# Kernel optimization log

Measured on AMD Instinct MI355X. Metric: run time of the kernel, lower is better.

Reference implementation:

```python
import jax, jax.numpy as jnp
import numpy as np

B = 256      # graph pairs
N = 256      # nodes per graph (uniform -> padding is a reshape)
DEG = 16     # avg degree
D = 32       # one_hot_dim
F1, F2, F3 = 128, 64, 64
T = 16       # tensor_neurons
BINS = 16
BOT = 16     # bottle_neck_neurons


def setup_inputs() -> dict:
    key = jax.random.key(0)
    ks = jax.random.split(key, 24)
    NT = B * N            # total nodes per side
    NE = B * N * DEG      # total directed edges per side
    x_q = jax.random.normal(ks[0], (NT, D), jnp.float32)
    x_c = jax.random.normal(ks[1], (NT, D), jnp.float32)
    edge_q = jax.random.randint(ks[2], (2, NE), 0, NT, jnp.int32)
    edge_c = jax.random.randint(ks[3], (2, NE), 0, NT, jnp.int32)
    qgraph_sizes = jnp.full((B,), N, jnp.int32)
    cgraph_sizes = jnp.full((B,), N, jnp.int32)

    def glorot(k, shape):
        fan = sum(shape[-2:]) if len(shape) >= 2 else shape[0] * 2
        return jax.random.uniform(k, shape, jnp.float32, -1.0, 1.0) * np.sqrt(6.0 / fan)

    params = dict(
        W1=glorot(ks[4], (D, F1)), b1=jnp.zeros((F1,), jnp.float32),
        W2=glorot(ks[5], (F1, F2)), b2=jnp.zeros((F2,), jnp.float32),
        W3=glorot(ks[6], (F2, F3)), b3=jnp.zeros((F3,), jnp.float32),
        attn_w=glorot(ks[7], (F3, F3)),
        ntn_a_w=glorot(ks[8], (T, F3, F3)),
        ntn_b_w=glorot(ks[9], (2 * F3, T)),
        ntn_bias=glorot(ks[10], (T, 1)),
        fc1_w=glorot(ks[11], (T + BINS, BOT)), fc1_b=jnp.zeros((BOT,), jnp.float32),
        fc2_w=glorot(ks[12], (BOT, 1)), fc2_b=jnp.zeros((1,), jnp.float32),
    )
    return dict(x_q=x_q, edge_q=edge_q, x_c=x_c, edge_c=edge_c,
                qgraph_sizes=qgraph_sizes, cgraph_sizes=cgraph_sizes, **params)


def _gcn(x, src, dst, W, b):
    n = x.shape[0]
    h = x @ W
    loop = jnp.arange(n, dtype=src.dtype)
    s = jnp.concatenate([src, loop])
    d = jnp.concatenate([dst, loop])
    deg = jax.ops.segment_sum(jnp.ones(s.shape, h.dtype), d, num_segments=n)
    dinv = jnp.where(deg > 0, jax.lax.rsqrt(jnp.maximum(deg, 1.0)), 0.0)
    coef = (dinv[s] * dinv[d])[:, None]
    return jax.ops.segment_sum(h[s] * coef, d, num_segments=n) + b


def _gnn(x, ei, W1, b1, W2, b2, W3, b3):
    src, dst = ei[0], ei[1]
    h = jax.nn.relu(_gcn(x, src, dst, W1, b1))        # dropout is identity in eval
    h = jax.nn.relu(_gcn(h, src, dst, W2, b2))
    return _gcn(h, src, dst, W3, b3)                  # [B*N, F3]


def _att_pool(q, attn_w, sizes):
    # q: [B, N, F3]
    ctx = jnp.tanh((q.sum(axis=1) @ attn_w) / sizes.astype(q.dtype)[:, None])  # [B, F3]
    sig = jax.nn.sigmoid(jnp.einsum('bnf,bf->bn', q, ctx))                      # [B, N]
    return jnp.einsum('bnf,bn->bf', q, sig)                                     # [B, F3]


def _pair_hist(q, c):
    # per-pair histogram of q @ c^T with BINS bins over each pair's [min, max]
    s = jax.lax.stop_gradient(jnp.einsum('bnf,bmf->bnm', q, c))  # [B, N, N]
    mn = s.min(axis=(1, 2), keepdims=True)
    mx = s.max(axis=(1, 2), keepdims=True)
    idx = jnp.clip(jnp.floor((s - mn) / jnp.maximum(mx - mn, 1e-12) * BINS),
                   0, BINS - 1).astype(jnp.int32)
    gid = (idx + jnp.arange(B, dtype=jnp.int32)[:, None, None] * BINS).reshape(-1)
    h = jax.ops.segment_sum(jnp.ones(gid.shape, jnp.float32), gid,
                            num_segments=B * BINS).reshape(B, BINS)
    return h / h.sum(axis=1, keepdims=True)


def reference(x_q, edge_q, x_c, edge_c, qgraph_sizes, cgraph_sizes,
              W1, b1, W2, b2, W3, b3, attn_w, ntn_a_w, ntn_b_w, ntn_bias,
              fc1_w, fc1_b, fc2_w, fc2_b):
    q = _gnn(x_q, edge_q, W1, b1, W2, b2, W3, b3).reshape(B, N, F3)
    c = _gnn(x_c, edge_c, W1, b1, W2, b2, W3, b3).reshape(B, N, F3)
    e1 = _att_pool(q, attn_w, qgraph_sizes)
    e2 = _att_pool(c, attn_w, cgraph_sizes)
    ntn = (jnp.einsum('bi,tij,bj->bt', e1, ntn_a_w, e2)
           + jnp.concatenate([e1, e2], axis=-1) @ ntn_b_w
           + ntn_bias[:, 0])
    scores = jax.nn.relu(ntn)                                   # [B, T]
    hist = _pair_hist(q, c)                                     # [B, BINS]
    scores = jnp.concatenate([scores, hist], axis=1)
    scores = jax.nn.relu(scores @ fc1_w + fc1_b)
    p = jax.nn.sigmoid(scores @ fc2_w + fc2_b)[:, 0]            # [B]
    ged = -0.5 * (qgraph_sizes + cgraph_sizes).astype(p.dtype) * jnp.log(p)
    return ged
```

## Files before the change

### kernel.cpp

```cpp
#include <hip/hip_runtime.h>
#include <hip/hip_bf16.h>
#include <math.h>

#define BB 256
#define NN 256
#define NT (BB*NN)
#define NT2 (2*NT)
#define NE (NT*16)
#define DD 32
#define F1C 128
#define F2C 64
#define F3C 64
#define TT 16
#define BINS 16

#define NBUCK 256
#define BSHIFT 9
#define BNODES 512
#define BCAP 10240
#define EPB 4096

typedef __attribute__((ext_vector_type(8))) short short8;
typedef __attribute__((ext_vector_type(4))) float f32x4;
typedef __attribute__((ext_vector_type(2))) float f32x2;

__device__ inline float b2f(ushort u) { return __uint_as_float(((uint)u) << 16); }
__device__ inline ushort f2b(float f) {
    uint u = __float_as_uint(f);
    return (ushort)((u + 0x7fffu + ((u >> 16) & 1u)) >> 16);
}
__device__ inline float clamp8(float v) { return fminf(fmaxf(v, -448.0f), 448.0f); }
__device__ inline uchar f2f8(float v) {
    int r = __builtin_amdgcn_cvt_pk_fp8_f32(clamp8(v), 0.0f, 0, false);
    return (uchar)(r & 0xff);
}
__device__ inline void f8x8_acc(uint2 w, float* acc) {
    f32x2 p;
    p = __builtin_amdgcn_cvt_pk_f32_fp8(w.x, false); acc[0] += p.x; acc[1] += p.y;
    p = __builtin_amdgcn_cvt_pk_f32_fp8(w.x, true);  acc[2] += p.x; acc[3] += p.y;
    p = __builtin_amdgcn_cvt_pk_f32_fp8(w.y, false); acc[4] += p.x; acc[5] += p.y;
    p = __builtin_amdgcn_cvt_pk_f32_fp8(w.y, true);  acc[6] += p.x; acc[7] += p.y;
}
__device__ inline uint2 f8x8_pack(const float* v) {
    uint2 r;
    r.x = (uint)__builtin_amdgcn_cvt_pk_fp8_f32(clamp8(v[0]), clamp8(v[1]), 0, false);
    r.x = (uint)__builtin_amdgcn_cvt_pk_fp8_f32(clamp8(v[2]), clamp8(v[3]), (int)r.x, true);
    r.y = (uint)__builtin_amdgcn_cvt_pk_fp8_f32(clamp8(v[4]), clamp8(v[5]), 0, false);
    r.y = (uint)__builtin_amdgcn_cvt_pk_fp8_f32(clamp8(v[6]), clamp8(v[7]), (int)r.y, true);
    return r;
}

__global__ __launch_bounds__(256) void zero_k(int* __restrict__ gcount) {
    gcount[threadIdx.x] = 0;
}

__global__ __launch_bounds__(256) void p1cvt_k(const int* __restrict__ eq, const int* __restrict__ ec,
                                               uint* __restrict__ staged, int* __restrict__ gcount,
                                               const float* __restrict__ W1, const float* __restrict__ W2,
                                               const float* __restrict__ W3, ushort* __restrict__ Wt1,
                                               ushort* __restrict__ Wt2, uchar* __restrict__ Wt3f8) {
    int t = threadIdx.x;
    if (blockIdx.x < 512) {
        __shared__ uint s_pk[EPB];
        __shared__ int s_cnt[NBUCK];
        __shared__ int s_off[NBUCK];
        __shared__ int s_base[NBUCK];
        __shared__ int s_gb[NBUCK];
        bool sideB = blockIdx.x >= 256;
        const int* edge = sideB ? ec : eq;
        int off = sideB ? NT : 0;
        int e0 = (blockIdx.x & 255) * EPB;
        s_cnt[t] = 0;
        __syncthreads();
        uint pk[16]; int bk[16];
#pragma unroll
        for (int j = 0; j < 16; j++) {
            int e = e0 + j * 256 + t;
            int s = edge[e] + off;
            int d = edge[NE + e] + off;
            bk[j] = d >> BSHIFT;
            pk[j] = ((uint)s << BSHIFT) | (uint)(d & (BNODES - 1));
            atomicAdd(&s_cnt[bk[j]], 1);
        }
        __syncthreads();
        s_off[t] = s_cnt[t];
        __syncthreads();
        for (int o = 1; o < NBUCK; o <<= 1) {
            int x = (t >= o) ? s_off[t - o] : 0;
            __syncthreads();
            s_off[t] += x;
            __syncthreads();
        }
        {
            int ex = s_off[t] - s_cnt[t];
            s_base[t] = ex;
            s_off[t] = ex;
            s_gb[t] = atomicAdd(&gcount[t], s_cnt[t]);
        }
        __syncthreads();
#pragma unroll
        for (int j = 0; j < 16; j++) {
            int pos = atomicAdd(&s_off[bk[j]], 1);
            s_pk[pos] = pk[j];
        }
        __syncthreads();
        int w = t >> 6, l = t & 63;
        int bsel = l >> 4, l16 = l & 15;
        for (int pb = w; pb < NBUCK / 4; pb += 4) {
            int bkt = pb * 4 + bsel;
            int n = s_cnt[bkt], st = s_base[bkt], gb = s_gb[bkt];
            if (gb + n > BCAP) n = max(0, BCAP - gb);
            for (int i = l16; i < n; i += 16)
                staged[bkt * BCAP + gb + i] = s_pk[st + i];
        }
    } else {
        int i = (blockIdx.x - 512) * 256 + t;
        if (i < DD * F1C)  { int k = i / F1C, n = i % F1C; Wt1[n * DD + k]  = f2b(W1[i]); }
        if (i < F1C * F2C) { int k = i / F2C, n = i % F2C; Wt2[n * F1C + k] = f2b(W2[i]); }
        if (i < F2C * F3C) { int k = i / F3C, n = i % F3C; Wt3f8[n * F2C + k] = f2f8(W3[i]); }
    }
}

__global__ __launch_bounds__(256) void csr_p2_k(const uint* __restrict__ staged, const int* __restrict__ gcount,
                                                int* __restrict__ rp, int* __restrict__ indeg,
                                                float* __restrict__ dinv, int* __restrict__ ep,
                                                const float* __restrict__ xq, const float* __restrict__ xc,
                                                ushort* __restrict__ xb) {
    int b = blockIdx.x;
    int t = threadIdx.x;
    __shared__ int cnt[BNODES];
    __shared__ int fl[BNODES];
    __shared__ int wsum[256];
    __shared__ int gsc[NBUCK];
    __shared__ float sdv[BNODES];
    cnt[t] = 0; cnt[t + 256] = 0;
    gsc[t] = min(gcount[t], BCAP);
    __syncthreads();
    for (int off = 1; off < NBUCK; off <<= 1) {
        int x = (t >= off) ? gsc[t - off] : 0;
        __syncthreads();
        gsc[t] += x;
        __syncthreads();
    }
    int gbase = (b == 0) ? 0 : gsc[b - 1];
    int n = min(gcount[b], BCAP);
    const uint* sb = staged + (size_t)b * BCAP;
    int i = t;
    for (; i + 768 < n; i += 1024) {
        uint p0 = sb[i];
        uint p1 = sb[i + 256];
        uint p2 = sb[i + 512];
        uint p3 = sb[i + 768];
        atomicAdd(&cnt[p0 & (BNODES - 1)], 1);
        atomicAdd(&cnt[p1 & (BNODES - 1)], 1);
        atomicAdd(&cnt[p2 & (BNODES - 1)], 1);
        atomicAdd(&cnt[p3 & (BNODES - 1)], 1);
    }
    for (; i < n; i += 256)
        atomicAdd(&cnt[sb[i] & (BNODES - 1)], 1);
    __syncthreads();
    int base2 = t * 2;
    int c0 = cnt[base2], c1 = cnt[base2 + 1];
    int s2 = c0 + c1;
    wsum[t] = s2;
    __syncthreads();
    for (int off = 1; off < 256; off <<= 1) {
        int x = (t >= off) ? wsum[t - off] : 0;
        __syncthreads();
        wsum[t] += x;
        __syncthreads();
    }
    int p = gbase + wsum[t] - s2;
    int v0 = b * BNODES + base2;
    float d0 = rsqrtf((float)(c0 + 1));
    float d1 = rsqrtf((float)(c1 + 1));
    rp[v0] = p;          fl[base2] = p;
    indeg[v0] = c0;      dinv[v0] = d0;      sdv[base2] = d0;
    p += c0;
    rp[v0 + 1] = p;      fl[base2 + 1] = p;
    indeg[v0 + 1] = c1;  dinv[v0 + 1] = d1;  sdv[base2 + 1] = d1;
    __syncthreads();
    i = t;
    for (; i + 768 < n; i += 1024) {
        uint p0 = sb[i];
        uint p1 = sb[i + 256];
        uint p2 = sb[i + 512];
        uint p3 = sb[i + 768];
        ep[atomicAdd(&fl[p0 & (BNODES - 1)], 1)] = (int)(p0 >> BSHIFT);
        ep[atomicAdd(&fl[p1 & (BNODES - 1)], 1)] = (int)(p1 >> BSHIFT);
        ep[atomicAdd(&fl[p2 & (BNODES - 1)], 1)] = (int)(p2 >> BSHIFT);
        ep[atomicAdd(&fl[p3 & (BNODES - 1)], 1)] = (int)(p3 >> BSHIFT);
    }
    for (; i < n; i += 256) {
        uint pk = sb[i];
        ep[atomicAdd(&fl[pk & (BNODES - 1)], 1)] = (int)(pk >> BSHIFT);
    }
    {
        const float* xs = (b < 128) ? (xq + (size_t)b * BNODES * DD)
                                    : (xc + ((size_t)b * BNODES - NT) * DD);
        ushort* xd = xb + (size_t)b * BNODES * DD;
        for (int g = t; g < BNODES * DD / 4; g += 256) {
            int r = g >> 3;
            float4 v = ((const float4*)xs)[g];
            float dv = sdv[r];
            ushort4 o;
            o.x = f2b(v.x * dv); o.y = f2b(v.y * dv);
            o.z = f2b(v.z * dv); o.w = f2b(v.w * dv);
            ((ushort4*)xd)[g] = o;
        }
    }
}

__global__ __launch_bounds__(256) void l1_k(const ushort* __restrict__ xb,
                                            const ushort* __restrict__ Wt1,
                                            const float* __restrict__ b1,
                                            const ushort* __restrict__ Wt2,
                                            const int* __restrict__ rp,
                                            const int* __restrict__ indeg,
                                            const int* __restrict__ ep,
                                            const float* __restrict__ dinv,
                                            uchar* __restrict__ h8a) {
    __shared__ ushort s_x[64][40];
    __shared__ ushort s_h1[64][136];
    int t = threadIdx.x;
    size_t rows0 = (size_t)blockIdx.x * 64;

    {
        int gl = t >> 2;
        int l4 = t & 3;
        int v = (int)rows0 + gl;
        float dv = dinv[v];
        short8 rs = *(const short8*)(xb + (size_t)v * 32 + l4 * 8);
        float acc[8];
#pragma unroll
        for (int j = 0; j < 8; j++) acc[j] = b2f((ushort)rs[j]);
        int start = rp[v];
        int cnt   = indeg[v];
        int i = 0;
        for (; i + 8 <= cnt; i += 8) {
            int sx[8];
#pragma unroll
            for (int j = 0; j < 8; j++) sx[j] = ep[start + i + j];
            short8 r[8];
#pragma unroll
            for (int j = 0; j < 8; j++) r[j] = *(const short8*)(xb + (size_t)sx[j] * 32 + l4 * 8);
#pragma unroll
            for (int j = 0; j < 8; j++)
#pragma unroll
                for (int k = 0; k < 8; k++) acc[k] += b2f((ushort)r[j][k]);
        }
        for (; i < cnt; i++) {
            int s0 = ep[start + i];
            short8 r0 = *(const short8*)(xb + (size_t)s0 * 32 + l4 * 8);
#pragma unroll
            for (int j = 0; j < 8; j++) acc[j] += b2f((ushort)r0[j]);
        }
        short8 o;
#pragma unroll
        for (int j = 0; j < 8; j++) o[j] = (short)f2b(dv * acc[j]);
        *(short8*)&s_x[gl][l4 * 8] = o;
    }
    __syncthreads();

    int w = t >> 6, lane = t & 63;
    int r16 = lane & 15, quad = lane >> 4, koff = quad * 8;

    short8 af1 = *(const short8*)&s_x[w * 16 + r16][koff];
#pragma unroll
    for (int nt = 0; nt < 8; nt++) {
        short8 bfr = *(const short8*)(Wt1 + (size_t)(nt * 16 + r16) * 32 + koff);
        f32x4 acc = {0.f, 0.f, 0.f, 0.f};
        acc = __builtin_amdgcn_mfma_f32_16x16x32_bf16(af1, bfr, acc, 0, 0, 0);
        int col = nt * 16 + r16;
        float bc = b1[col];
#pragma unroll
        for (int r = 0; r < 4; r++) {
            int rl = w * 16 + quad * 4 + r;
            s_h1[rl][col] = f2b(fmaxf(acc[r] + bc, 0.0f));
        }
    }
    __syncthreads();

    short8 af2[4];
#pragma unroll
    for (int kc = 0; kc < 4; kc++)
        af2[kc] = *(const short8*)&s_h1[w * 16 + r16][kc * 32 + koff];
    float dvr[4];
#pragma unroll
    for (int r = 0; r < 4; r++)
        dvr[r] = dinv[rows0 + w * 16 + quad * 4 + r];
#pragma unroll
    for (int nt = 0; nt < 4; nt++) {
        f32x4 acc = {0.f, 0.f, 0.f, 0.f};
#pragma unroll
        for (int kc = 0; kc < 4; kc++) {
            short8 bfr = *(const short8*)(Wt2 + (size_t)(nt * 16 + r16) * 128 + kc * 32 + koff);
            acc = __builtin_amdgcn_mfma_f32_16x16x32_bf16(af2[kc], bfr, acc, 0, 0, 0);
        }
#pragma unroll
        for (int r = 0; r < 4; r++) {
            size_t row = rows0 + w * 16 + quad * 4 + r;
            int col = nt * 16 + r16;
            h8a[row * 64 + col] = f2f8(acc[r] * dvr[r]);
        }
    }
}

__global__ __launch_bounds__(256) void l2_k(const uchar* __restrict__ in,
                                            const int* __restrict__ rp,
                                            const int* __restrict__ indeg,
                                            const int* __restrict__ ep,
                                            const float* __restrict__ dinv,
                                            const float* __restrict__ b2,
                                            const uchar* __restrict__ Wt8,
                                            uchar* __restrict__ out8) {
    __shared__ uchar s_a[64][72];
    int t = threadIdx.x;
    size_t rows0 = (size_t)blockIdx.x * 64;

    int g8 = t >> 3;
    int l8 = t & 7;
#pragma unroll
    for (int pass = 0; pass < 2; pass++) {
        int vloc = pass * 32 + g8;
        int v = (int)rows0 + vloc;
        float dv = dinv[v];
        float acc[8] = {0, 0, 0, 0, 0, 0, 0, 0};
        f8x8_acc(*(const uint2*)(in + (size_t)v * 64 + l8 * 8), acc);
        int start = rp[v];
        int cnt   = indeg[v];
        int i = 0;
        for (; i + 8 <= cnt; i += 8) {
            int sx[8];
#pragma unroll
            for (int j = 0; j < 8; j++) sx[j] = ep[start + i + j];
            uint2 gx[8];
#pragma unroll
            for (int j = 0; j < 8; j++) gx[j] = *(const uint2*)(in + (size_t)sx[j] * 64 + l8 * 8);
#pragma unroll
            for (int j = 0; j < 8; j++) f8x8_acc(gx[j], acc);
        }
        for (; i < cnt; i++) {
            int s0 = ep[start + i];
            f8x8_acc(*(const uint2*)(in + (size_t)s0 * 64 + l8 * 8), acc);
        }
#pragma unroll
        for (int j = 0; j < 8; j++)
            acc[j] = fmaxf(dv * acc[j] + b2[l8 * 8 + j], 0.0f);
        *(uint2*)&s_a[vloc][l8 * 8] = f8x8_pack(acc);
    }
    __syncthreads();

    int w = t >> 6, lane = t & 63;
    int r16 = lane & 15, koff = (lane >> 4) * 8;

    long af[2];
#pragma unroll
    for (int kc = 0; kc < 2; kc++)
        af[kc] = *(const long*)&s_a[w * 16 + r16][kc * 32 + koff];

    float dvr[4];
#pragma unroll
    for (int r = 0; r < 4; r++)
        dvr[r] = dinv[rows0 + w * 16 + (lane >> 4) * 4 + r];

#pragma unroll
    for (int nt = 0; nt < 4; nt++) {
        f32x4 acc = {0.f, 0.f, 0.f, 0.f};
#pragma unroll
        for (int kc = 0; kc < 2; kc++) {
            long b = *(const long*)(Wt8 + (size_t)(nt * 16 + r16) * 64 + kc * 32 + koff);
            acc = __builtin_amdgcn_mfma_f32_16x16x32_fp8_fp8(af[kc], b, acc, 0, 0, 0);
        }
#pragma unroll
        for (int r = 0; r < 4; r++) {
            size_t row = rows0 + w * 16 + (lane >> 4) * 4 + r;
            int col = nt * 16 + (lane & 15);
            out8[row * 64 + col] = f2f8(acc[r] * dvr[r]);
        }
    }
}

template<bool OUT_BF16, bool BIAS, bool RELU>
__global__ __launch_bounds__(256) void agg_f8_k(const uchar* __restrict__ in, const int* __restrict__ rp,
                                                const int* __restrict__ indeg, const int* __restrict__ ep,
                                                const float* __restrict__ dinv,
                                                const float* __restrict__ bias, void* __restrict__ outp) {
    int g = threadIdx.x >> 3;
    int l = threadIdx.x & 7;
    int v = blockIdx.x * 32 + g;
    float dv = dinv[v];
    float acc[8] = {0, 0, 0, 0, 0, 0, 0, 0};
    f8x8_acc(*(const uint2*)(in + (size_t)v * 64 + l * 8), acc);
    int start = rp[v];
    int cnt   = indeg[v];
    int i = 0;
    for (; i + 8 <= cnt; i += 8) {
        int sx[8];
#pragma unroll
        for (int j = 0; j < 8; j++) sx[j] = ep[start + i + j];
        uint2 gx[8];
#pragma unroll
        for (int j = 0; j < 8; j++) gx[j] = *(const uint2*)(in + (size_t)sx[j] * 64 + l * 8);
#pragma unroll
        for (int j = 0; j < 8; j++) f8x8_acc(gx[j], acc);
    }
    for (; i + 4 <= cnt; i += 4) {
        int s0 = ep[start + i];
        int s1 = ep[start + i + 1];
        int s2 = ep[start + i + 2];
        int s3 = ep[start + i + 3];
        uint2 g0 = *(const uint2*)(in + (size_t)s0 * 64 + l * 8);
        uint2 g1 = *(const uint2*)(in + (size_t)s1 * 64 + l * 8);
        uint2 g2 = *(const uint2*)(in + (size_t)s2 * 64 + l * 8);
        uint2 g3 = *(const uint2*)(in + (size_t)s3 * 64 + l * 8);
        f8x8_acc(g0, acc); f8x8_acc(g1, acc); f8x8_acc(g2, acc); f8x8_acc(g3, acc);
    }
    for (; i < cnt; i++) {
        int s0 = ep[start + i];
        f8x8_acc(*(const uint2*)(in + (size_t)s0 * 64 + l * 8), acc);
    }
#pragma unroll
    for (int j = 0; j < 8; j++) {
        float x = dv * acc[j];
        if (BIAS) x += bias[l * 8 + j];
        if (RELU) x = fmaxf(x, 0.0f);
        acc[j] = x;
    }
    if (OUT_BF16) {
        short8 o;
#pragma unroll
        for (int j = 0; j < 8; j++) o[j] = (short)f2b(acc[j]);
        *(short8*)((ushort*)outp + (size_t)v * 64 + l * 8) = o;
    } else {
        *(uint2*)((uchar*)outp + (size_t)v * 64 + l * 8) = f8x8_pack(acc);
    }
}

__global__ __launch_bounds__(256) void pool_hist_k(const ushort* __restrict__ fin,
                                                   const int* __restrict__ qsz, const int* __restrict__ csz,
                                                   const float* __restrict__ attn_w,
                                                   float* __restrict__ e_out, float* __restrict__ histp) {
    __shared__ float smemf[17472];
    int t = threadIdx.x;
    if (blockIdx.x < 512) {
        int b = blockIdx.x & 255;
        bool is_c = blockIdx.x >= BB;
        const ushort* emb = fin + (size_t)blockIdx.x * NN * F3C;
        float size = (float)((is_c ? csz : qsz)[b]);
        float* eo = e_out + (is_c ? BB * F3C : 0) + b * F3C;
        float (*s_emb)[F3C + 1] = (float(*)[F3C + 1])smemf;
        float* s_red = smemf + 256 * 65;
        float* s_sq  = s_red + 256;
        float* s_ctx = s_sq + 64;
        float* s_sig = s_ctx + 64;
        int f = t & 63;
        int w = t >> 6;
#pragma unroll
        for (int it = 0; it < 8; it++) {
            int idx = it * 2048 + t * 8;
            int row = idx >> 6, f0 = idx & 63;
            short8 v = *(const short8*)(emb + idx);
#pragma unroll
            for (int j = 0; j < 8; j++) s_emb[row][f0 + j] = b2f((ushort)v[j]);
        }
        __syncthreads();
        float psum = 0.0f;
#pragma unroll 8
        for (int i2 = 0; i2 < 64; i2++) psum += s_emb[w * 64 + i2][f];
        s_red[w * 64 + f] = psum;
        __syncthreads();
        if (w == 0) {
            s_sq[f] = s_red[f] + s_red[64 + f] + s_red[128 + f] + s_red[192 + f];
            float acc = 0.0f;
            for (int k = 0; k < 64; k++) acc += s_sq[k] * attn_w[k * 64 + f];
            s_ctx[f] = tanhf(acc / size);
        }
        __syncthreads();
        {
            float acc = 0.0f;
#pragma unroll 8
            for (int k = 0; k < 64; k++) acc += s_emb[t][k] * s_ctx[k];
            s_sig[t] = 1.0f / (1.0f + expf(-acc));
        }
        __syncthreads();
        float eacc = 0.0f;
#pragma unroll 8
        for (int i = 0; i < 64; i++) {
            int n = w * 64 + i;
            eacc += s_sig[n] * s_emb[n][f];
        }
        s_red[w * 64 + f] = eacc;
        __syncthreads();
        if (w == 0) eo[f] = s_red[f] + s_red[64 + f] + s_red[128 + f] + s_red[192 + f];
    } else {
        int b = blockIdx.x - 512;
        const ushort* qb = fin + (size_t)b * NN * 64;
        const ushort* cb = fin + (size_t)(NT + b * NN) * 64;
        int lane = t & 63;
        int w = t >> 6;
        int r16 = lane & 15, koff = (lane >> 4) * 8;
        ushort (*cb_s)[72] = (ushort(*)[72])smemf;
        int* h = (int*)(smemf + 9216);
        int* hp = h + 16 * 256;
        float* smn = (float*)(hp + 256);
        float* smx = smn + 4;
        float* s_sc = smx + 4;

#pragma unroll
        for (int it = 0; it < 8; it++) {
            int idx = it * 2048 + t * 8;
            int row = idx >> 6, f0 = idx & 63;
            *(short8*)&cb_s[row][f0] = *(const short8*)(cb + idx);
        }
        short8 a[4][2];
#pragma unroll
        for (int i = 0; i < 4; i++) {
            int row = (w * 4 + i) * 16 + r16;
#pragma unroll
            for (int kk = 0; kk < 2; kk++)
                a[i][kk] = *(const short8*)(qb + row * 64 + kk * 32 + koff);
        }
        __syncthreads();
        float mn = 1e30f, mx = -1e30f;
        for (int mt = 0; mt < 16; mt++) {
            int crow = mt * 16 + r16;
            short8 b0 = *(const short8*)&cb_s[crow][koff];
            short8 b1 = *(const short8*)&cb_s[crow][32 + koff];
#pragma unroll
            for (int i = 0; i < 4; i++) {
                f32x4 acc = {0.0f, 0.0f, 0.0f, 0.0f};
                acc = __builtin_amdgcn_mfma_f32_16x16x32_bf16(a[i][0], b0, acc, 0, 0, 0);
                acc = __builtin_amdgcn_mfma_f32_16x16x32_bf16(a[i][1], b1, acc, 0, 0, 0);
                mn = fminf(mn, fminf(fminf(acc[0], acc[1]), fminf(acc[2], acc[3])));
                mx = fmaxf(mx, fmaxf(fmaxf(acc[0], acc[1]), fmaxf(acc[2], acc[3])));
            }
        }
        for (int off = 32; off; off >>= 1) {
            mn = fminf(mn, __shfl_xor(mn, off, 64));
            mx = fmaxf(mx, __shfl_xor(mx, off, 64));
        }
        if (lane == 0) { smn[w] = mn; smx[w] = mx; }
        __syncthreads();
        if (t == 0) {
            float m0 = fminf(fminf(smn[0], smn[1]), fminf(smn[2], smn[3]));
            float m1 = fmaxf(fmaxf(smx[0], smx[1]), fmaxf(smx[2], smx[3]));
            s_sc[0] = m0;
            s_sc[1] = 16.0f / fmaxf(m1 - m0, 1e-12f);
        }
#pragma unroll
        for (int i = 0; i < 16; i++) h[i * 256 + t] = 0;
        __syncthreads();
        float bmn = s_sc[0], bscale = s_sc[1];
        for (int mt = 0; mt < 16; mt++) {
            int crow = mt * 16 + r16;
            short8 b0 = *(const short8*)&cb_s[crow][koff];
            short8 b1 = *(const short8*)&cb_s[crow][32 + koff];
#pragma unroll
            for (int i = 0; i < 4; i++) {
                f32x4 acc = {0.0f, 0.0f, 0.0f, 0.0f};
                acc = __builtin_amdgcn_mfma_f32_16x16x32_bf16(a[i][0], b0, acc, 0, 0, 0);
                acc = __builtin_amdgcn_mfma_f32_16x16x32_bf16(a[i][1], b1, acc, 0, 0, 0);
#pragma unroll
                for (int r = 0; r < 4; r++) {
                    int bin = (int)floorf((acc[r] - bmn) * bscale);
                    bin = min(max(bin, 0), 15);
                    h[bin * 256 + t] += 1;
                }
            }
        }
        __syncthreads();
        int bb = t >> 4, part = t & 15;
        int sum = 0;
#pragma unroll
        for (int j = 0; j < 16; j++) sum += h[bb * 256 + part * 16 + j];
        hp[bb * 16 + part] = sum;
        __syncthreads();
        if (t < 16) {
            int s = 0;
#pragma unroll
            for (int j = 0; j < 16; j++) s += hp[t * 16 + j];
            histp[b * 16 + t] = (float)s;
        }
    }
}

__global__ __launch_bounds__(256) void ntn_final_k(const float* __restrict__ e, const float* __restrict__ A,
                                                   const float* __restrict__ bw, const float* __restrict__ bias,
                                                   const float* __restrict__ histp,
                                                   const float* __restrict__ fc1w, const float* __restrict__ fc1b,
                                                   const float* __restrict__ fc2w, const float* __restrict__ fc2b,
                                                   const int* __restrict__ qsz, const int* __restrict__ csz,
                                                   float* __restrict__ out) {
    int b = blockIdx.x;
    int t = threadIdx.x;
    int lane = t & 63, w = t >> 6;
    __shared__ float s_e1[64], s_e2[64];
    __shared__ float s_ntn[16];
    __shared__ float s_s[32];
    __shared__ float s_a[16];
    if (t < 64) s_e1[t] = e[b * 64 + t];
    else if (t < 128) s_e2[t - 64] = e[BB * 64 + b * 64 + (t - 64)];
    __syncthreads();
#pragma unroll
    for (int r = 0; r < 4; r++) {
        int idx = t + r * 256;
        const float4* Ar = (const float4*)(A + (size_t)idx * 64);
        float acc = 0.0f;
#pragma unroll
        for (int j = 0; j < 16; j++) {
            float4 a4 = Ar[j];
            acc += a4.x * s_e2[4 * j] + a4.y * s_e2[4 * j + 1]
                 + a4.z * s_e2[4 * j + 2] + a4.w * s_e2[4 * j + 3];
        }
        float p = s_e1[lane] * acc;
        for (int off = 32; off; off >>= 1) p += __shfl_xor(p, off, 64);
        if (lane == 0) s_ntn[w + 4 * r] = p;
    }
    __syncthreads();
    if (t < 16) {
        float acc = s_ntn[t] + bias[t];
        for (int k = 0; k < 64; k++) acc += s_e1[k] * bw[k * 16 + t];
        for (int k = 0; k < 64; k++) acc += s_e2[k] * bw[(64 + k) * 16 + t];
        s_s[t] = fmaxf(acc, 0.0f);
        s_s[16 + t] = histp[b * 16 + t] * (1.0f / 65536.0f);
    }
    __syncthreads();
    if (t < 16) {
        float a = fc1b[t];
        for (int k = 0; k < 32; k++) a += s_s[k] * fc1w[k * 16 + t];
        s_a[t] = fmaxf(a, 0.0f);
    }
    __syncthreads();
    if (t == 0) {
        float z = fc2b[0];
        for (int j = 0; j < 16; j++) z += s_a[j] * fc2w[j];
        float nz = -z;
        float sp = (nz > 20.0f) ? nz : log1pf(expf(nz));
        out[b] = 0.5f * (float)(qsz[b] + csz[b]) * sp;
    }
}

extern "C" void kernel_launch(void* const* d_in, const int* in_sizes, int n_in,
                              void* d_out, int out_size, void* d_ws, size_t ws_size,
                              hipStream_t stream) {
    const float* x_q    = (const float*)d_in[0];
    const int*   edge_q = (const int*)d_in[1];
    const float* x_c    = (const float*)d_in[2];
    const int*   edge_c = (const int*)d_in[3];
    const int*   qsz    = (const int*)d_in[4];
    const int*   csz    = (const int*)d_in[5];
    const float* W1 = (const float*)d_in[6];
    const float* b1 = (const float*)d_in[7];
    const float* W2 = (const float*)d_in[8];
    const float* b2 = (const float*)d_in[9];
    const float* W3 = (const float*)d_in[10];
    const float* b3 = (const float*)d_in[11];
    const float* attn_w  = (const float*)d_in[12];
    const float* ntn_a   = (const float*)d_in[13];
    const float* ntn_b   = (const float*)d_in[14];
    const float* ntn_bias= (const float*)d_in[15];
    const float* fc1w = (const float*)d_in[16];
    const float* fc1b = (const float*)d_in[17];
    const float* fc2w = (const float*)d_in[18];
    const float* fc2b = (const float*)d_in[19];
    float* out = (float*)d_out;

    char* w = (char*)d_ws;
    auto alloc = [&](size_t bytes) -> void* {
        void* p = (void*)w;
        w += (bytes + 255) & ~(size_t)255;
        return p;
    };
    int*    rp     = (int*)alloc((size_t)NT2 * 4);
    int*    indeg  = (int*)alloc((size_t)NT2 * 4);
    float*  dinv   = (float*)alloc((size_t)NT2 * 4);
    int*    gcount = (int*)alloc(NBUCK * 4);
    uint*   staged = (uint*)alloc((size_t)NBUCK * BCAP * 4);
    int*    ep     = (int*)alloc((size_t)2 * NE * 4);
    ushort* xb     = (ushort*)alloc((size_t)NT2 * 32 * 2);
    uchar*  h8a    = (uchar*)alloc((size_t)NT2 * 64);
    uchar*  h8b    = (uchar*)alloc((size_t)NT2 * 64);
    ushort* fin    = (ushort*)alloc((size_t)NT2 * 64 * 2);
    ushort* Wt1    = (ushort*)alloc((size_t)DD * F1C * 2);
    ushort* Wt2    = (ushort*)alloc((size_t)F1C * F2C * 2);
    uchar*  Wt3f8  = (uchar*)alloc((size_t)F2C * F3C);
    float*  e12    = (float*)alloc(2 * BB * 64 * 4);
    float*  histp  = (float*)alloc(256 * 16 * 4);

    zero_k<<<1, 256, 0, stream>>>(gcount);
    p1cvt_k<<<512 + 32, 256, 0, stream>>>(edge_q, edge_c, staged, gcount,
                                          W1, W2, W3, Wt1, Wt2, Wt3f8);
    csr_p2_k<<<NBUCK, 256, 0, stream>>>(staged, gcount, rp, indeg, dinv, ep,
                                        x_q, x_c, xb);

    l1_k<<<NT2 / 64, 256, 0, stream>>>(xb, Wt1, b1, Wt2, rp, indeg, ep, dinv, h8a);
    l2_k<<<NT2 / 64, 256, 0, stream>>>(h8a, rp, indeg, ep, dinv, b2, Wt3f8, h8b);
    agg_f8_k<true, true, false><<<NT2 / 32, 256, 0, stream>>>(h8b, rp, indeg, ep, dinv, b3, fin);

    pool_hist_k<<<768, 256, 0, stream>>>(fin, qsz, csz, attn_w, e12, histp);
    ntn_final_k<<<BB, 256, 0, stream>>>(e12, ntn_a, ntn_b, ntn_bias, histp,
                                        fc1w, fc1b, fc2w, fc2b, qsz, csz, out);
}
```

Baseline: 291.4 us.

## Split GCN features into column halves and unfuse gathers from GEMMs

Node features are stored as two separate column-half arrays, so each neighbour-gather pass touches only 32-byte rows and has a smaller cache footprint. Gather kernels are pulled out of the MFMA GEMM kernels, and each layer now runs one gather per half followed by a GEMM that reads both halves. Edge-index loads and output stores are marked nontemporal. The cost is that the edge list is read twice per layer, more kernels are launched, and extra intermediate buffers are written to and read from global memory.

```diff
diff --git a/kernel.cpp b/kernel.cpp
--- a/kernel.cpp
+++ b/kernel.cpp
@@ -23,6 +23,7 @@
 typedef __attribute__((ext_vector_type(8))) short short8;
 typedef __attribute__((ext_vector_type(4))) float f32x4;
 typedef __attribute__((ext_vector_type(2))) float f32x2;
+typedef __attribute__((ext_vector_type(4))) uint u32x4;
 
 __device__ inline float b2f(ushort u) { return __uint_as_float(((uint)u) << 16); }
 __device__ inline ushort f2b(float f) {
@@ -34,12 +35,13 @@
     int r = __builtin_amdgcn_cvt_pk_fp8_f32(clamp8(v), 0.0f, 0, false);
     return (uchar)(r & 0xff);
 }
+__device__ inline void f8w_acc(uint w, float* acc) {
+    f32x2 p;
+    p = __builtin_amdgcn_cvt_pk_f32_fp8(w, false); acc[0] += p.x; acc[1] += p.y;
+    p = __builtin_amdgcn_cvt_pk_f32_fp8(w, true);  acc[2] += p.x; acc[3] += p.y;
+}
 __device__ inline void f8x8_acc(uint2 w, float* acc) {
-    f32x2 p;
-    p = __builtin_amdgcn_cvt_pk_f32_fp8(w.x, false); acc[0] += p.x; acc[1] += p.y;
-    p = __builtin_amdgcn_cvt_pk_f32_fp8(w.x, true);  acc[2] += p.x; acc[3] += p.y;
-    p = __builtin_amdgcn_cvt_pk_f32_fp8(w.y, false); acc[4] += p.x; acc[5] += p.y;
-    p = __builtin_amdgcn_cvt_pk_f32_fp8(w.y, true);  acc[6] += p.x; acc[7] += p.y;
+    f8w_acc(w.x, acc); f8w_acc(w.y, acc + 4);
 }
 __device__ inline uint2 f8x8_pack(const float* v) {
     uint2 r;
@@ -47,6 +49,15 @@
     r.x = (uint)__builtin_amdgcn_cvt_pk_fp8_f32(clamp8(v[2]), clamp8(v[3]), (int)r.x, true);
     r.y = (uint)__builtin_amdgcn_cvt_pk_fp8_f32(clamp8(v[4]), clamp8(v[5]), 0, false);
     r.y = (uint)__builtin_amdgcn_cvt_pk_fp8_f32(clamp8(v[6]), clamp8(v[7]), (int)r.y, true);
+    return r;
+}
+__device__ inline void f8x16_acc(u32x4 w, float* acc) {
+    f8w_acc(w[0], acc); f8w_acc(w[1], acc + 4);
+    f8w_acc(w[2], acc + 8); f8w_acc(w[3], acc + 12);
+}
+__device__ inline u32x4 f8x16_pack(const float* v) {
+    uint2 a = f8x8_pack(v); uint2 b = f8x8_pack(v + 8);
+    u32x4 r; r[0] = a.x; r[1] = a.y; r[2] = b.x; r[3] = b.y;
     return r;
 }
 
@@ -125,7 +136,7 @@
                                                 int* __restrict__ rp, int* __restrict__ indeg,
                                                 float* __restrict__ dinv, int* __restrict__ ep,
                                                 const float* __restrict__ xq, const float* __restrict__ xc,
-                                                ushort* __restrict__ xb) {
+                                                ushort* __restrict__ xb0, ushort* __restrict__ xb1) {
     int b = blockIdx.x;
     int t = threadIdx.x;
     __shared__ int cnt[BNODES];
@@ -198,74 +209,149 @@
     {
         const float* xs = (b < 128) ? (xq + (size_t)b * BNODES * DD)
                                     : (xc + ((size_t)b * BNODES - NT) * DD);
-        ushort* xd = xb + (size_t)b * BNODES * DD;
         for (int g = t; g < BNODES * DD / 4; g += 256) {
             int r = g >> 3;
+            int dg = g & 7;
             float4 v = ((const float4*)xs)[g];
             float dv = sdv[r];
             ushort4 o;
             o.x = f2b(v.x * dv); o.y = f2b(v.y * dv);
             o.z = f2b(v.z * dv); o.w = f2b(v.w * dv);
-            ((ushort4*)xd)[g] = o;
-        }
-    }
-}
-
-__global__ __launch_bounds__(256) void l1_k(const ushort* __restrict__ xb,
-                                            const ushort* __restrict__ Wt1,
-                                            const float* __restrict__ b1,
-                                            const ushort* __restrict__ Wt2,
-                                            const int* __restrict__ rp,
-                                            const int* __restrict__ indeg,
-                                            const int* __restrict__ ep,
-                                            const float* __restrict__ dinv,
-                                            uchar* __restrict__ h8a) {
-    __shared__ ushort s_x[64][40];
+            ushort* dst = ((dg < 4) ? xb0 : xb1) + ((size_t)(b * BNODES + r)) * 16 + (dg & 3) * 4;
+            *(ushort4*)dst = o;
+        }
+    }
+}
+
+__global__ __launch_bounds__(256) void aggp_bf_k(const ushort* __restrict__ in,
+                                                 const int* __restrict__ rp,
+                                                 const int* __restrict__ indeg,
+                                                 const int* __restrict__ ep,
+                                                 const float* __restrict__ dinv,
+                                                 ushort* __restrict__ out) {
+    int t = threadIdx.x;
+    int v = blockIdx.x * 128 + (t >> 1);
+    int l = t & 1;
+    float dv = dinv[v];
+    short8 rs = *(const short8*)(in + (size_t)v * 16 + l * 8);
+    float acc[8];
+#pragma unroll
+    for (int j = 0; j < 8; j++) acc[j] = b2f((ushort)rs[j]);
+    int start = rp[v];
+    int cnt   = indeg[v];
+    int i = 0;
+    for (; i + 8 <= cnt; i += 8) {
+        int sx[8];
+#pragma unroll
+        for (int j = 0; j < 8; j++) sx[j] = __builtin_nontemporal_load(ep + start + i + j);
+        short8 r[8];
+#pragma unroll
+        for (int j = 0; j < 8; j++) r[j] = *(const short8*)(in + (size_t)sx[j] * 16 + l * 8);
+#pragma unroll
+        for (int j = 0; j < 8; j++)
+#pragma unroll
+            for (int k = 0; k < 8; k++) acc[k] += b2f((ushort)r[j][k]);
+    }
+    for (; i + 4 <= cnt; i += 4) {
+        int sx[4];
+#pragma unroll
+        for (int j = 0; j < 4; j++) sx[j] = __builtin_nontemporal_load(ep + start + i + j);
+        short8 r[4];
+#pragma unroll
+        for (int j = 0; j < 4; j++) r[j] = *(const short8*)(in + (size_t)sx[j] * 16 + l * 8);
+#pragma unroll
+        for (int j = 0; j < 4; j++)
+#pragma unroll
+            for (int k = 0; k < 8; k++) acc[k] += b2f((ushort)r[j][k]);
+    }
+    for (; i < cnt; i++) {
+        int s0 = __builtin_nontemporal_load(ep + start + i);
+        short8 r0 = *(const short8*)(in + (size_t)s0 * 16 + l * 8);
+#pragma unroll
+        for (int j = 0; j < 8; j++) acc[j] += b2f((ushort)r0[j]);
+    }
+    short8 o;
+#pragma unroll
+    for (int j = 0; j < 8; j++) o[j] = (short)f2b(dv * acc[j]);
+    __builtin_nontemporal_store(o, (short8*)(out + (size_t)v * 16 + l * 8));
+}
+
+template<bool RELU, bool OUT_BF16>
+__global__ __launch_bounds__(256) void aggp_f8_k(const uchar* __restrict__ in,
+                                                 const int* __restrict__ rp,
+                                                 const int* __restrict__ indeg,
+                                                 const int* __restrict__ ep,
+                                                 const float* __restrict__ dinv,
+                                                 const float* __restrict__ bias,
+                                                 void* __restrict__ outp) {
+    int t = threadIdx.x;
+    int v = blockIdx.x * 128 + (t >> 1);
+    int l = t & 1;
+    float dv = dinv[v];
+    float acc[16] = {0,0,0,0,0,0,0,0,0,0,0,0,0,0,0,0};
+    f8x16_acc(*(const u32x4*)(in + (size_t)v * 32 + l * 16), acc);
+    int start = rp[v];
+    int cnt   = indeg[v];
+    int i = 0;
+    for (; i + 8 <= cnt; i += 8) {
+        int sx[8];
+#pragma unroll
+        for (int j = 0; j < 8; j++) sx[j] = __builtin_nontemporal_load(ep + start + i + j);
+        u32x4 gx[8];
+#pragma unroll
+        for (int j = 0; j < 8; j++) gx[j] = *(const u32x4*)(in + (size_t)sx[j] * 32 + l * 16);
+#pragma unroll
+        for (int j = 0; j < 8; j++) f8x16_acc(gx[j], acc);
+    }
+    for (; i + 4 <= cnt; i += 4) {
+        int sx[4];
+#pragma unroll
+        for (int j = 0; j < 4; j++) sx[j] = __builtin_nontemporal_load(ep + start + i + j);
+        u32x4 gx[4];
+#pragma unroll
+        for (int j = 0; j < 4; j++) gx[j] = *(const u32x4*)(in + (size_t)sx[j] * 32 + l * 16);
+#pragma unroll
+        for (int j = 0; j < 4; j++) f8x16_acc(gx[j], acc);
+    }
+    for (; i < cnt; i++) {
+        int s0 = __builtin_nontemporal_load(ep + start + i);
+        f8x16_acc(*(const u32x4*)(in + (size_t)s0 * 32 + l * 16), acc);
+    }
+#pragma unroll
+    for (int j = 0; j < 16; j++) {
+        float x = dv * acc[j] + bias[l * 16 + j];
+        if (RELU) x = fmaxf(x, 0.0f);
+        acc[j] = x;
+    }
+    if (OUT_BF16) {
+        ushort* ob = (ushort*)outp + (size_t)v * 64 + l * 16;
+        short8 o0, o1;
+#pragma unroll
+        for (int j = 0; j < 8; j++) { o0[j] = (short)f2b(acc[j]); o1[j] = (short)f2b(acc[8 + j]); }
+        __builtin_nontemporal_store(o0, (short8*)ob);
+        __builtin_nontemporal_store(o1, (short8*)(ob + 8));
+    } else {
+        __builtin_nontemporal_store(f8x16_pack(acc),
+                                    (u32x4*)((uchar*)outp + (size_t)v * 32 + l * 16));
+    }
+}
+
+__global__ __launch_bounds__(256) void gemm12_k(const ushort* __restrict__ sx0,
+                                                const ushort* __restrict__ sx1,
+                                                const ushort* __restrict__ Wt1,
+                                                const float* __restrict__ b1,
+                                                const ushort* __restrict__ Wt2,
+                                                const float* __restrict__ dinv,
+                                                uchar* __restrict__ ha0, uchar* __restrict__ ha1) {
     __shared__ ushort s_h1[64][136];
     int t = threadIdx.x;
-    size_t rows0 = (size_t)blockIdx.x * 64;
-
-    {
-        int gl = t >> 2;
-        int l4 = t & 3;
-        int v = (int)rows0 + gl;
-        float dv = dinv[v];
-        short8 rs = *(const short8*)(xb + (size_t)v * 32 + l4 * 8);
-        float acc[8];
-#pragma unroll
-        for (int j = 0; j < 8; j++) acc[j] = b2f((ushort)rs[j]);
-        int start = rp[v];
-        int cnt   = indeg[v];
-        int i = 0;
-        for (; i + 8 <= cnt; i += 8) {
-            int sx[8];
-#pragma unroll
-            for (int j = 0; j < 8; j++) sx[j] = ep[start + i + j];
-            short8 r[8];
-#pragma unroll
-            for (int j = 0; j < 8; j++) r[j] = *(const short8*)(xb + (size_t)sx[j] * 32 + l4 * 8);
-#pragma unroll
-            for (int j = 0; j < 8; j++)
-#pragma unroll
-                for (int k = 0; k < 8; k++) acc[k] += b2f((ushort)r[j][k]);
-        }
-        for (; i < cnt; i++) {
-            int s0 = ep[start + i];
-            short8 r0 = *(const short8*)(xb + (size_t)s0 * 32 + l4 * 8);
-#pragma unroll
-            for (int j = 0; j < 8; j++) acc[j] += b2f((ushort)r0[j]);
-        }
-        short8 o;
-#pragma unroll
-        for (int j = 0; j < 8; j++) o[j] = (short)f2b(dv * acc[j]);
-        *(short8*)&s_x[gl][l4 * 8] = o;
-    }
-    __syncthreads();
-
     int w = t >> 6, lane = t & 63;
     int r16 = lane & 15, quad = lane >> 4, koff = quad * 8;
-
-    short8 af1 = *(const short8*)&s_x[w * 16 + r16][koff];
+    size_t rows0 = (size_t)blockIdx.x * 64;
+    size_t arow = rows0 + w * 16 + r16;
+
+    const ushort* pl = (quad < 2) ? sx0 : sx1;
+    short8 af1 = *(const short8*)(pl + arow * 16 + (quad & 1) * 8);
 #pragma unroll
     for (int nt = 0; nt < 8; nt++) {
         short8 bfr = *(const short8*)(Wt1 + (size_t)(nt * 16 + r16) * 32 + koff);
@@ -297,67 +383,30 @@
             short8 bfr = *(const short8*)(Wt2 + (size_t)(nt * 16 + r16) * 128 + kc * 32 + koff);
             acc = __builtin_amdgcn_mfma_f32_16x16x32_bf16(af2[kc], bfr, acc, 0, 0, 0);
         }
+        uchar* hp = (nt < 2) ? ha0 : ha1;
+        int coln = (nt & 1) * 16 + r16;
 #pragma unroll
         for (int r = 0; r < 4; r++) {
             size_t row = rows0 + w * 16 + quad * 4 + r;
-            int col = nt * 16 + r16;
-            h8a[row * 64 + col] = f2f8(acc[r] * dvr[r]);
-        }
-    }
-}
-
-__global__ __launch_bounds__(256) void l2_k(const uchar* __restrict__ in,
-                                            const int* __restrict__ rp,
-                                            const int* __restrict__ indeg,
-                                            const int* __restrict__ ep,
-                                            const float* __restrict__ dinv,
-                                            const float* __restrict__ b2,
-                                            const uchar* __restrict__ Wt8,
-                                            uchar* __restrict__ out8) {
-    __shared__ uchar s_a[64][72];
+            hp[row * 32 + coln] = f2f8(acc[r] * dvr[r]);
+        }
+    }
+}
+
+__global__ __launch_bounds__(256) void gemm3_k(const uchar* __restrict__ ga0,
+                                               const uchar* __restrict__ ga1,
+                                               const uchar* __restrict__ Wt8,
+                                               const float* __restrict__ dinv,
+                                               uchar* __restrict__ hb0, uchar* __restrict__ hb1) {
     int t = threadIdx.x;
-    size_t rows0 = (size_t)blockIdx.x * 64;
-
-    int g8 = t >> 3;
-    int l8 = t & 7;
-#pragma unroll
-    for (int pass = 0; pass < 2; pass++) {
-        int vloc = pass * 32 + g8;
-        int v = (int)rows0 + vloc;
-        float dv = dinv[v];
-        float acc[8] = {0, 0, 0, 0, 0, 0, 0, 0};
-        f8x8_acc(*(const uint2*)(in + (size_t)v * 64 + l8 * 8), acc);
-        int start = rp[v];
-        int cnt   = indeg[v];
-        int i = 0;
-        for (; i + 8 <= cnt; i += 8) {
-            int sx[8];
-#pragma unroll
-            for (int j = 0; j < 8; j++) sx[j] = ep[start + i + j];
-            uint2 gx[8];
-#pragma unroll
-            for (int j = 0; j < 8; j++) gx[j] = *(const uint2*)(in + (size_t)sx[j] * 64 + l8 * 8);
-#pragma unroll
-            for (int j = 0; j < 8; j++) f8x8_acc(gx[j], acc);
-        }
-        for (; i < cnt; i++) {
-            int s0 = ep[start + i];
-            f8x8_acc(*(const uint2*)(in + (size_t)s0 * 64 + l8 * 8), acc);
-        }
-#pragma unroll
-        for (int j = 0; j < 8; j++)
-            acc[j] = fmaxf(dv * acc[j] + b2[l8 * 8 + j], 0.0f);
-        *(uint2*)&s_a[vloc][l8 * 8] = f8x8_pack(acc);
-    }
-    __syncthreads();
-
     int w = t >> 6, lane = t & 63;
     int r16 = lane & 15, koff = (lane >> 4) * 8;
+    size_t rows0 = (size_t)blockIdx.x * 64;
+    size_t arow = rows0 + w * 16 + r16;
 
     long af[2];
-#pragma unroll
-    for (int kc = 0; kc < 2; kc++)
-        af[kc] = *(const long*)&s_a[w * 16 + r16][kc * 32 + koff];
+    af[0] = *(const long*)(ga0 + arow * 32 + koff);
+    af[1] = *(const long*)(ga1 + arow * 32 + koff);
 
     float dvr[4];
 #pragma unroll
@@ -372,68 +421,13 @@
             long b = *(const long*)(Wt8 + (size_t)(nt * 16 + r16) * 64 + kc * 32 + koff);
             acc = __builtin_amdgcn_mfma_f32_16x16x32_fp8_fp8(af[kc], b, acc, 0, 0, 0);
         }
+        uchar* hp = (nt < 2) ? hb0 : hb1;
+        int coln = (nt & 1) * 16 + r16;
 #pragma unroll
         for (int r = 0; r < 4; r++) {
             size_t row = rows0 + w * 16 + (lane >> 4) * 4 + r;
-            int col = nt * 16 + (lane & 15);
-            out8[row * 64 + col] = f2f8(acc[r] * dvr[r]);
-        }
-    }
-}
-
-template<bool OUT_BF16, bool BIAS, bool RELU>
-__global__ __launch_bounds__(256) void agg_f8_k(const uchar* __restrict__ in, const int* __restrict__ rp,
-                                                const int* __restrict__ indeg, const int* __restrict__ ep,
-                                                const float* __restrict__ dinv,
-                                                const float* __restrict__ bias, void* __restrict__ outp) {
-    int g = threadIdx.x >> 3;
-    int l = threadIdx.x & 7;
-    int v = blockIdx.x * 32 + g;
-    float dv = dinv[v];
-    float acc[8] = {0, 0, 0, 0, 0, 0, 0, 0};
-    f8x8_acc(*(const uint2*)(in + (size_t)v * 64 + l * 8), acc);
-    int start = rp[v];
-    int cnt   = indeg[v];
-    int i = 0;
-    for (; i + 8 <= cnt; i += 8) {
-        int sx[8];
-#pragma unroll
-        for (int j = 0; j < 8; j++) sx[j] = ep[start + i + j];
-        uint2 gx[8];
-#pragma unroll
-        for (int j = 0; j < 8; j++) gx[j] = *(const uint2*)(in + (size_t)sx[j] * 64 + l * 8);
-#pragma unroll
-        for (int j = 0; j < 8; j++) f8x8_acc(gx[j], acc);
-    }
-    for (; i + 4 <= cnt; i += 4) {
-        int s0 = ep[start + i];
-        int s1 = ep[start + i + 1];
-        int s2 = ep[start + i + 2];
-        int s3 = ep[start + i + 3];
-        uint2 g0 = *(const uint2*)(in + (size_t)s0 * 64 + l * 8);
-        uint2 g1 = *(const uint2*)(in + (size_t)s1 * 64 + l * 8);
-        uint2 g2 = *(const uint2*)(in + (size_t)s2 * 64 + l * 8);
-        uint2 g3 = *(const uint2*)(in + (size_t)s3 * 64 + l * 8);
-        f8x8_acc(g0, acc); f8x8_acc(g1, acc); f8x8_acc(g2, acc); f8x8_acc(g3, acc);
-    }
-    for (; i < cnt; i++) {
-        int s0 = ep[start + i];
-        f8x8_acc(*(const uint2*)(in + (size_t)s0 * 64 + l * 8), acc);
-    }
-#pragma unroll
-    for (int j = 0; j < 8; j++) {
-        float x = dv * acc[j];
-        if (BIAS) x += bias[l * 8 + j];
-        if (RELU) x = fmaxf(x, 0.0f);
-        acc[j] = x;
-    }
-    if (OUT_BF16) {
-        short8 o;
-#pragma unroll
-        for (int j = 0; j < 8; j++) o[j] = (short)f2b(acc[j]);
-        *(short8*)((ushort*)outp + (size_t)v * 64 + l * 8) = o;
-    } else {
-        *(uint2*)((uchar*)outp + (size_t)v * 64 + l * 8) = f8x8_pack(acc);
+            hp[row * 32 + coln] = f2f8(acc[r] * dvr[r]);
+        }
     }
 }
 
@@ -678,9 +672,16 @@
     int*    gcount = (int*)alloc(NBUCK * 4);
     uint*   staged = (uint*)alloc((size_t)NBUCK * BCAP * 4);
     int*    ep     = (int*)alloc((size_t)2 * NE * 4);
-    ushort* xb     = (ushort*)alloc((size_t)NT2 * 32 * 2);
-    uchar*  h8a    = (uchar*)alloc((size_t)NT2 * 64);
-    uchar*  h8b    = (uchar*)alloc((size_t)NT2 * 64);
+    ushort* xb0    = (ushort*)alloc((size_t)NT2 * 16 * 2);
+    ushort* xb1    = (ushort*)alloc((size_t)NT2 * 16 * 2);
+    ushort* sx0    = (ushort*)alloc((size_t)NT2 * 16 * 2);
+    ushort* sx1    = (ushort*)alloc((size_t)NT2 * 16 * 2);
+    uchar*  ha0    = (uchar*)alloc((size_t)NT2 * 32);
+    uchar*  ha1    = (uchar*)alloc((size_t)NT2 * 32);
+    uchar*  ga0    = (uchar*)alloc((size_t)NT2 * 32);
+    uchar*  ga1    = (uchar*)alloc((size_t)NT2 * 32);
+    uchar*  hb0    = (uchar*)alloc((size_t)NT2 * 32);
+    uchar*  hb1    = (uchar*)alloc((size_t)NT2 * 32);
     ushort* fin    = (ushort*)alloc((size_t)NT2 * 64 * 2);
     ushort* Wt1    = (ushort*)alloc((size_t)DD * F1C * 2);
     ushort* Wt2    = (ushort*)alloc((size_t)F1C * F2C * 2);
@@ -692,11 +693,16 @@
     p1cvt_k<<<512 + 32, 256, 0, stream>>>(edge_q, edge_c, staged, gcount,
                                           W1, W2, W3, Wt1, Wt2, Wt3f8);
     csr_p2_k<<<NBUCK, 256, 0, stream>>>(staged, gcount, rp, indeg, dinv, ep,
-                                        x_q, x_c, xb);
-
-    l1_k<<<NT2 / 64, 256, 0, stream>>>(xb, Wt1, b1, Wt2, rp, indeg, ep, dinv, h8a);
-    l2_k<<<NT2 / 64, 256, 0, stream>>>(h8a, rp, indeg, ep, dinv, b2, Wt3f8, h8b);
-    agg_f8_k<true, true, false><<<NT2 / 32, 256, 0, stream>>>(h8b, rp, indeg, ep, dinv, b3, fin);
+                                        x_q, x_c, xb0, xb1);
+
+    aggp_bf_k<<<NT2 / 128, 256, 0, stream>>>(xb0, rp, indeg, ep, dinv, sx0);
+    aggp_bf_k<<<NT2 / 128, 256, 0, stream>>>(xb1, rp, indeg, ep, dinv, sx1);
+    gemm12_k<<<NT2 / 64, 256, 0, stream>>>(sx0, sx1, Wt1, b1, Wt2, dinv, ha0, ha1);
+    aggp_f8_k<true, false><<<NT2 / 128, 256, 0, stream>>>(ha0, rp, indeg, ep, dinv, b2, ga0);
+    aggp_f8_k<true, false><<<NT2 / 128, 256, 0, stream>>>(ha1, rp, indeg, ep, dinv, b2 + 32, ga1);
+    gemm3_k<<<NT2 / 64, 256, 0, stream>>>(ga0, ga1, Wt3f8, dinv, hb0, hb1);
+    aggp_f8_k<false, true><<<NT2 / 128, 256, 0, stream>>>(hb0, rp, indeg, ep, dinv, b3, fin);
+    aggp_f8_k<false, true><<<NT2 / 128, 256, 0, stream>>>(hb1, rp, indeg, ep, dinv, b3 + 32, fin + 32);
 
     pool_hist_k<<<768, 256, 0, stream>>>(fin, qsz, csz, attn_w, e12, histp);
     ntn_final_k<<<BB, 256, 0, stream>>>(e12, ntn_a, ntn_b, ntn_bias, histp,
```

Measured after the change: 371.4 us. 27.4% more time.
